# Performance work log

Hardware: AMD Instinct MI355X
Metric: run time of the kernel (lower is better)

The kernel has to match this reference:

```python
import jax, jax.numpy as jnp
import numpy as np

NUM_USERS = 100000
NUM_ITEMS = 50000
DIM = 128
NUM_EDGES = 600000


def setup_inputs() -> dict:
    key = jax.random.key(0)
    k1, k2, k3, k4, k5, k6 = jax.random.split(key, 6)
    u_emb = jax.random.normal(k1, (NUM_USERS, DIM), dtype=jnp.float32)
    i_emb = jax.random.normal(k2, (NUM_ITEMS, DIM), dtype=jnp.float32)
    user_idx = jax.random.randint(k3, (NUM_EDGES,), 0, NUM_USERS, dtype=jnp.int32)
    item_idx = jax.random.randint(k4, (NUM_EDGES,), 0, NUM_ITEMS, dtype=jnp.int32)
    edge_index = jnp.stack([user_idx, item_idx], axis=0)
    # weights in [0.2, 1.0] per docstring (unused in eval-mode forward)
    weights = 0.2 + 0.8 * jax.random.uniform(k5, (NUM_EDGES,), dtype=jnp.float32)
    attn_w = jax.random.normal(k6, (2 * DIM,), dtype=jnp.float32) * (1.0 / np.sqrt(2 * DIM))
    return {"u_emb": u_emb, "i_emb": i_emb, "edge_index": edge_index,
            "weights": weights, "attn_w": attn_w}


def _scatter_softmax(scores, idx, num_nodes):
    # numerically stable segment softmax over edges grouped by idx
    smax = jax.ops.segment_max(scores, idx, num_segments=num_nodes)  # [N]
    exp_s = jnp.exp(scores - smax[idx])                              # [E]
    ssum = jax.ops.segment_sum(exp_s, idx, num_segments=num_nodes)   # [N]
    return exp_s / (ssum[idx] + 1e-10)


def reference(u_emb, i_emb, edge_index, weights, attn_w):
    num_users = u_emb.shape[0]
    num_items = i_emb.shape[0]
    dim = u_emb.shape[1]
    user_idx, item_idx = edge_index[0], edge_index[1]

    # attn_projector(cat([u, i])) == u @ w_u + i @ w_i (no bias)
    w_u, w_i = attn_w[:dim], attn_w[dim:]
    raw = u_emb[user_idx] @ w_u + i_emb[item_idx] @ w_i  # [E]
    raw = jnp.where(raw >= 0, raw, 0.2 * raw)            # LeakyReLU(0.2)

    u_attn = _scatter_softmax(raw, user_idx, num_users)  # [E]
    i_attn = _scatter_softmax(raw, item_idx, num_items)  # [E]

    new_u = u_emb.at[user_idx].add(i_emb[item_idx] * u_attn[:, None])
    new_i = i_emb.at[item_idx].add(u_emb[user_idx] * i_attn[:, None])
    return new_u, new_i
```

## Files before the change

kernel.cpp:

```cpp
#include <hip/hip_runtime.h>

#define DIM 128
#define SCAN_BLK 1024

__device__ __forceinline__ unsigned short bf16rn(float f) {
    unsigned u = __float_as_uint(f);
    u += 0x7fffu + ((u >> 16) & 1u);
    return (unsigned short)(u >> 16);
}

__global__ void k_prep(const float* __restrict__ u_emb, const float* __restrict__ i_emb,
                       const float* __restrict__ attn_w, float* __restrict__ sdot,
                       ushort2* __restrict__ bemb, int nu, int n, int do_bf16) {
    int gw = (blockIdx.x * blockDim.x + threadIdx.x) >> 6;
    int lane = threadIdx.x & 63;
    if (gw >= n) return;
    const bool isU = gw < nu;
    const float2* row = (const float2*)(isU ? u_emb + (size_t)gw * DIM
                                            : i_emb + (size_t)(gw - nu) * DIM);
    const float2* wv  = (const float2*)(isU ? attn_w : attn_w + DIM);
    float2 a = row[lane];
    float2 b = wv[lane];
    float v = a.x * b.x + a.y * b.y;
    #pragma unroll
    for (int off = 32; off; off >>= 1) v += __shfl_down(v, off);
    if (lane == 0) sdot[gw] = v;
    if (do_bf16) {
        ushort2 h;
        h.x = bf16rn(a.x);
        h.y = bf16rn(a.y);
        bemb[(size_t)gw * (DIM / 2) + lane] = h;
    }
}

__global__ void k_count(const int* __restrict__ uidx, const int* __restrict__ iidx,
                        unsigned* __restrict__ cnt, unsigned* __restrict__ ranks,
                        int nu, int ne) {
    int e = blockIdx.x * blockDim.x + threadIdx.x;
    if (e >= ne) return;
    unsigned r0 = atomicAdd(&cnt[uidx[e]], 1u);
    unsigned r1 = atomicAdd(&cnt[nu + iidx[e]], 1u);
    ranks[e] = (r0 << 16) | (r1 & 0xffffu);
}

__global__ void k_scan1(const unsigned* __restrict__ cnt, unsigned* __restrict__ incl,
                        unsigned* __restrict__ bsum, int n) {
    __shared__ unsigned part[SCAN_BLK];
    int t = threadIdx.x;
    int j = blockIdx.x * SCAN_BLK + t;
    unsigned v = (j < n) ? cnt[j] : 0u;
    part[t] = v;
    __syncthreads();
    for (int d = 1; d < SCAN_BLK; d <<= 1) {
        unsigned w = (t >= d) ? part[t - d] : 0u;
        __syncthreads();
        part[t] += w;
        __syncthreads();
    }
    if (j < n) incl[j] = part[t];
    if (t == SCAN_BLK - 1) bsum[blockIdx.x] = part[t];
}

__global__ void k_scan2(unsigned* __restrict__ bsum, int nb) {
    __shared__ unsigned part[SCAN_BLK];
    int t = threadIdx.x;
    unsigned v = (t < nb) ? bsum[t] : 0u;
    part[t] = v;
    __syncthreads();
    for (int d = 1; d < SCAN_BLK; d <<= 1) {
        unsigned w = (t >= d) ? part[t - d] : 0u;
        __syncthreads();
        part[t] += w;
        __syncthreads();
    }
    if (t < nb) bsum[t] = part[t] - v;
}

__global__ void k_scan3(const unsigned* __restrict__ cnt, const unsigned* __restrict__ incl,
                        const unsigned* __restrict__ bsum,
                        unsigned* __restrict__ off, int n) {
    int j = blockIdx.x * blockDim.x + threadIdx.x;
    if (j >= n) return;
    off[j] = incl[j] - cnt[j] + bsum[j / SCAN_BLK];
}

__global__ void k_edge(const int* __restrict__ uidx, const int* __restrict__ iidx,
                       const float* __restrict__ sdot, const unsigned* __restrict__ off,
                       const unsigned* __restrict__ ranks,
                       unsigned long long* __restrict__ pairs,
                       int nu, int ne) {
    int e = blockIdx.x * blockDim.x + threadIdx.x;
    if (e >= ne) return;
    int u = uidx[e], i = iidx[e];
    float r = sdot[u] + sdot[nu + i];
    r = (r >= 0.f) ? r : 0.2f * r;
    float x = expf(r);
    unsigned long long hi = (unsigned long long)__float_as_uint(x) << 32;
    unsigned rk = ranks[e];
    pairs[off[u]      + (rk >> 16)]      = hi | (unsigned)i;
    pairs[off[nu + i] + (rk & 0xffffu)]  = hi | (unsigned)u;
}

template <int BF16>
__global__ void k_accum(const float* __restrict__ u_emb, const float* __restrict__ i_emb,
                        const ushort2* __restrict__ bemb,
                        const unsigned* __restrict__ off, const unsigned* __restrict__ cnt,
                        const unsigned long long* __restrict__ pairs,
                        float* __restrict__ out, int nu, int n) {
    int gw = (blockIdx.x * blockDim.x + threadIdx.x) >> 6;
    int lane = threadIdx.x & 63;
    if (gw >= n) return;
    const bool isUser = gw < nu;
    const float* self = isUser ? (u_emb + (size_t)gw * DIM)
                               : (i_emb + (size_t)(gw - nu) * DIM);
    const float* gBaseF = isUser ? i_emb : u_emb;
    const int gOfs = isUser ? nu : 0;
    float2 acc = make_float2(0.f, 0.f);
    float wsum = 0.f;
    unsigned s = off[gw];
    unsigned d = cnt[gw];

    auto fetch = [&](int o) -> float2 {
        if (BF16) {
            ushort2 h = bemb[(size_t)(gOfs + o) * (DIM / 2) + lane];
            return make_float2(__uint_as_float((unsigned)h.x << 16),
                               __uint_as_float((unsigned)h.y << 16));
        } else {
            return ((const float2*)(gBaseF + (size_t)o * DIM))[lane];
        }
    };

    unsigned j = 0;
    for (; j + 1 < d; j += 2) {
        unsigned long long p0 = pairs[s + j];
        unsigned long long p1 = pairs[s + j + 1];
        int o0 = (int)(p0 & 0xffffffffu);
        int o1 = (int)(p1 & 0xffffffffu);
        float w0 = __uint_as_float((unsigned)(p0 >> 32));
        float w1 = __uint_as_float((unsigned)(p1 >> 32));
        float2 v0 = fetch(o0);
        float2 v1 = fetch(o1);
        wsum += w0 + w1;
        acc.x += w0 * v0.x + w1 * v1.x;
        acc.y += w0 * v0.y + w1 * v1.y;
    }
    if (j < d) {
        unsigned long long p0 = pairs[s + j];
        int o0 = (int)(p0 & 0xffffffffu);
        float w0 = __uint_as_float((unsigned)(p0 >> 32));
        float2 v0 = fetch(o0);
        wsum += w0;
        acc.x += w0 * v0.x;
        acc.y += w0 * v0.y;
    }
    float inv = 1.f / (wsum + 1e-10f);
    float2 sv = ((const float2*)self)[lane];
    sv.x += acc.x * inv;
    sv.y += acc.y * inv;
    ((float2*)(out + (size_t)gw * DIM))[lane] = sv;
}

extern "C" void kernel_launch(void* const* d_in, const int* in_sizes, int n_in,
                              void* d_out, int out_size, void* d_ws, size_t ws_size,
                              hipStream_t stream) {
    const float* u_emb  = (const float*)d_in[0];
    const float* i_emb  = (const float*)d_in[1];
    const int*   edge   = (const int*)d_in[2];
    const float* attn_w = (const float*)d_in[4];

    const int nu = in_sizes[0] / DIM;
    const int ni = in_sizes[1] / DIM;
    const int ne = in_sizes[3];
    const int n  = nu + ni;

    const int* uidx = edge;
    const int* iidx = edge + ne;

    float* out = (float*)d_out;

    char* ws = (char*)d_ws;
    size_t used = 0;
    auto take = [&](size_t bytes) {
        char* p = ws + used;
        used += (bytes + 15) & ~size_t(15);
        return p;
    };
    float*    sdot  = (float*)   take((size_t)n * sizeof(float));
    unsigned* cnt   = (unsigned*)take((size_t)n * sizeof(unsigned));
    unsigned* off   = (unsigned*)take((size_t)n * sizeof(unsigned));
    unsigned* incl  = (unsigned*)take((size_t)n * sizeof(unsigned));
    unsigned* bsum  = (unsigned*)take((size_t)SCAN_BLK * sizeof(unsigned));
    unsigned* ranks = (unsigned*)take((size_t)ne * sizeof(unsigned));
    unsigned long long* pairs =
        (unsigned long long*)take((size_t)2 * ne * sizeof(unsigned long long));
    size_t bembBytes = (size_t)n * DIM * 2;
    const int do_bf16 = (used + bembBytes <= ws_size) ? 1 : 0;
    ushort2* bemb = do_bf16 ? (ushort2*)take(bembBytes) : (ushort2*)nullptr;

    const int nb = (n + SCAN_BLK - 1) / SCAN_BLK;

    hipMemsetAsync(cnt, 0, (size_t)n * sizeof(unsigned), stream);

    k_prep<<<(n + 3) / 4, 256, 0, stream>>>(u_emb, i_emb, attn_w, sdot, bemb, nu, n, do_bf16);

    k_count<<<(ne + 255) / 256, 256, 0, stream>>>(uidx, iidx, cnt, ranks, nu, ne);

    k_scan1<<<nb, SCAN_BLK, 0, stream>>>(cnt, incl, bsum, n);
    k_scan2<<<1, SCAN_BLK, 0, stream>>>(bsum, nb);
    k_scan3<<<(n + 255) / 256, 256, 0, stream>>>(cnt, incl, bsum, off, n);

    k_edge<<<(ne + 255) / 256, 256, 0, stream>>>(uidx, iidx, sdot, off, ranks, pairs, nu, ne);

    if (do_bf16)
        k_accum<1><<<(n + 3) / 4, 256, 0, stream>>>(u_emb, i_emb, bemb, off, cnt,
                                                    pairs, out, nu, n);
    else
        k_accum<0><<<(n + 3) / 4, 256, 0, stream>>>(u_emb, i_emb, bemb, off, cnt,
                                                    pairs, out, nu, n);
}
```

Measured before the change: 207.2 us.

## Move edge weight computation into accumulate kernel with wave-cooperative neighbor loads

```diff
diff --git a/kernel.cpp b/kernel.cpp
--- a/kernel.cpp
+++ b/kernel.cpp
@@ -84,76 +84,81 @@
     off[j] = incl[j] - cnt[j] + bsum[j / SCAN_BLK];
 }
 
-__global__ void k_edge(const int* __restrict__ uidx, const int* __restrict__ iidx,
-                       const float* __restrict__ sdot, const unsigned* __restrict__ off,
-                       const unsigned* __restrict__ ranks,
-                       unsigned long long* __restrict__ pairs,
-                       int nu, int ne) {
+__global__ void k_fill(const int* __restrict__ uidx, const int* __restrict__ iidx,
+                       const unsigned* __restrict__ off, const unsigned* __restrict__ ranks,
+                       int* __restrict__ nbr, int nu, int ne) {
     int e = blockIdx.x * blockDim.x + threadIdx.x;
     if (e >= ne) return;
     int u = uidx[e], i = iidx[e];
-    float r = sdot[u] + sdot[nu + i];
-    r = (r >= 0.f) ? r : 0.2f * r;
-    float x = expf(r);
-    unsigned long long hi = (unsigned long long)__float_as_uint(x) << 32;
     unsigned rk = ranks[e];
-    pairs[off[u]      + (rk >> 16)]      = hi | (unsigned)i;
-    pairs[off[nu + i] + (rk & 0xffffu)]  = hi | (unsigned)u;
+    nbr[off[u]      + (rk >> 16)]     = nu + i;
+    nbr[off[nu + i] + (rk & 0xffffu)] = u;
 }
 
 template <int BF16>
 __global__ void k_accum(const float* __restrict__ u_emb, const float* __restrict__ i_emb,
-                        const ushort2* __restrict__ bemb,
+                        const ushort2* __restrict__ bemb, const float* __restrict__ sdot,
                         const unsigned* __restrict__ off, const unsigned* __restrict__ cnt,
-                        const unsigned long long* __restrict__ pairs,
+                        const int* __restrict__ nbr,
                         float* __restrict__ out, int nu, int n) {
     int gw = (blockIdx.x * blockDim.x + threadIdx.x) >> 6;
     int lane = threadIdx.x & 63;
     if (gw >= n) return;
-    const bool isUser = gw < nu;
-    const float* self = isUser ? (u_emb + (size_t)gw * DIM)
-                               : (i_emb + (size_t)(gw - nu) * DIM);
-    const float* gBaseF = isUser ? i_emb : u_emb;
-    const int gOfs = isUser ? nu : 0;
+    float sd_self = sdot[gw];
+    unsigned s = off[gw];
+    unsigned d = cnt[gw];
     float2 acc = make_float2(0.f, 0.f);
     float wsum = 0.f;
-    unsigned s = off[gw];
-    unsigned d = cnt[gw];
 
     auto fetch = [&](int o) -> float2 {
         if (BF16) {
-            ushort2 h = bemb[(size_t)(gOfs + o) * (DIM / 2) + lane];
+            ushort2 h = bemb[(size_t)o * (DIM / 2) + lane];
             return make_float2(__uint_as_float((unsigned)h.x << 16),
                                __uint_as_float((unsigned)h.y << 16));
         } else {
-            return ((const float2*)(gBaseF + (size_t)o * DIM))[lane];
+            const float* base = (o < nu) ? u_emb + (size_t)o * DIM
+                                         : i_emb + (size_t)(o - nu) * DIM;
+            return ((const float2*)base)[lane];
         }
     };
 
-    unsigned j = 0;
-    for (; j + 1 < d; j += 2) {
-        unsigned long long p0 = pairs[s + j];
-        unsigned long long p1 = pairs[s + j + 1];
-        int o0 = (int)(p0 & 0xffffffffu);
-        int o1 = (int)(p1 & 0xffffffffu);
-        float w0 = __uint_as_float((unsigned)(p0 >> 32));
-        float w1 = __uint_as_float((unsigned)(p1 >> 32));
-        float2 v0 = fetch(o0);
-        float2 v1 = fetch(o1);
-        wsum += w0 + w1;
-        acc.x += w0 * v0.x + w1 * v1.x;
-        acc.y += w0 * v0.y + w1 * v1.y;
-    }
-    if (j < d) {
-        unsigned long long p0 = pairs[s + j];
-        int o0 = (int)(p0 & 0xffffffffu);
-        float w0 = __uint_as_float((unsigned)(p0 >> 32));
-        float2 v0 = fetch(o0);
-        wsum += w0;
-        acc.x += w0 * v0.x;
-        acc.y += w0 * v0.y;
-    }
+    for (unsigned base = 0; base < d; base += 64) {
+        unsigned chunk = d - base; if (chunk > 64) chunk = 64;
+        int   o = 0;
+        float w = 0.f;
+        if (lane < (int)chunk) {
+            o = nbr[s + base + lane];
+            float r = sd_self + sdot[o];
+            r = (r >= 0.f) ? r : 0.2f * r;
+            w = expf(r);
+        }
+        unsigned j = 0;
+        for (; j + 3 < chunk; j += 4) {
+            int   o0 = __shfl(o, (int)j),     o1 = __shfl(o, (int)j + 1);
+            int   o2 = __shfl(o, (int)j + 2), o3 = __shfl(o, (int)j + 3);
+            float w0 = __shfl(w, (int)j),     w1 = __shfl(w, (int)j + 1);
+            float w2 = __shfl(w, (int)j + 2), w3 = __shfl(w, (int)j + 3);
+            float2 v0 = fetch(o0);
+            float2 v1 = fetch(o1);
+            float2 v2 = fetch(o2);
+            float2 v3 = fetch(o3);
+            wsum += (w0 + w1) + (w2 + w3);
+            acc.x += w0 * v0.x + w1 * v1.x + w2 * v2.x + w3 * v3.x;
+            acc.y += w0 * v0.y + w1 * v1.y + w2 * v2.y + w3 * v3.y;
+        }
+        for (; j < chunk; ++j) {
+            int   oj = __shfl(o, (int)j);
+            float wj = __shfl(w, (int)j);
+            float2 vj = fetch(oj);
+            wsum += wj;
+            acc.x += wj * vj.x;
+            acc.y += wj * vj.y;
+        }
+    }
+
     float inv = 1.f / (wsum + 1e-10f);
+    const float* self = (gw < nu) ? u_emb + (size_t)gw * DIM
+                                  : i_emb + (size_t)(gw - nu) * DIM;
     float2 sv = ((const float2*)self)[lane];
     sv.x += acc.x * inv;
     sv.y += acc.y * inv;
@@ -191,8 +196,7 @@
     unsigned* incl  = (unsigned*)take((size_t)n * sizeof(unsigned));
     unsigned* bsum  = (unsigned*)take((size_t)SCAN_BLK * sizeof(unsigned));
     unsigned* ranks = (unsigned*)take((size_t)ne * sizeof(unsigned));
-    unsigned long long* pairs =
-        (unsigned long long*)take((size_t)2 * ne * sizeof(unsigned long long));
+    int*      nbr   = (int*)     take((size_t)2 * ne * sizeof(int));
     size_t bembBytes = (size_t)n * DIM * 2;
     const int do_bf16 = (used + bembBytes <= ws_size) ? 1 : 0;
     ushort2* bemb = do_bf16 ? (ushort2*)take(bembBytes) : (ushort2*)nullptr;
@@ -209,12 +213,12 @@
     k_scan2<<<1, SCAN_BLK, 0, stream>>>(bsum, nb);
     k_scan3<<<(n + 255) / 256, 256, 0, stream>>>(cnt, incl, bsum, off, n);
 
-    k_edge<<<(ne + 255) / 256, 256, 0, stream>>>(uidx, iidx, sdot, off, ranks, pairs, nu, ne);
+    k_fill<<<(ne + 255) / 256, 256, 0, stream>>>(uidx, iidx, off, ranks, nbr, nu, ne);
 
     if (do_bf16)
-        k_accum<1><<<(n + 3) / 4, 256, 0, stream>>>(u_emb, i_emb, bemb, off, cnt,
-                                                    pairs, out, nu, n);
+        k_accum<1><<<(n + 3) / 4, 256, 0, stream>>>(u_emb, i_emb, bemb, sdot, off, cnt,
+                                                    nbr, out, nu, n);
     else
-        k_accum<0><<<(n + 3) / 4, 256, 0, stream>>>(u_emb, i_emb, bemb, off, cnt,
-                                                    pairs, out, nu, n);
-}
+        k_accum<0><<<(n + 3) / 4, 256, 0, stream>>>(u_emb, i_emb, bemb, sdot, off, cnt,
+                                                    nbr, out, nu, n);
+}
```

Result: faster. 187.7 us (-9.4%).
